# Kernel tuning notes

Hardware: AMD Instinct MI355X
Metric: run time of the kernel (lower is better)

## Reference

```python
import jax, jax.numpy as jnp
import numpy as np

N = 256    # num_neurons
I = 784    # input_dim
H = 128    # hidden_dim
B = 256    # batch
E = 4096   # num edges (sparse topology, fan_out 16)


def setup_inputs() -> dict:
    key = jax.random.key(0)
    k0, k1, k2, k3, k4 = jax.random.split(key, 5)
    x = jax.random.normal(k0, (B, I), dtype=jnp.float32)
    # per-neuron linear weights/biases (AutonomicNeuron modeled as Linear(input_dim, hidden_dim))
    W = jax.random.normal(k1, (N, I, H), dtype=jnp.float32) * (1.0 / np.sqrt(I))
    b = jax.random.normal(k2, (N, H), dtype=jnp.float32) * 0.01
    edge_index = jax.random.randint(k3, (2, E), 0, N)  # (2, E) [src; tgt]
    edge_weights = jax.random.normal(k4, (E,), dtype=jnp.float32) * 0.01  # init scale in _init_*_topology
    return {"x": x, "W": W, "b": b, "edge_index": edge_index, "edge_weights": edge_weights}


def reference(x, W, b, edge_index, edge_weights):
    # per-neuron projection: h0[n] = x @ W[n] + b[n]  -> (N, B, H)
    h0 = jnp.einsum('bi,nih->nbh', x, W) + b[:, None, :]
    src = edge_index[0]
    tgt = edge_index[1]
    # sequential, order-dependent message passing (faithful to the Python edge loop):
    # h[tgt] <- h[tgt] + h[src] * w, using the CURRENT h[src]
    def step(h, sw):
        s, t, w = sw
        h = h.at[t].add(h[s] * w)
        return h, None
    h_final, _ = jax.lax.scan(step, h0, (src, tgt, edge_weights))
    # aggregate: mean over all neurons' hidden states -> (B, H)
    return h_final.mean(axis=0)
```

## Files before the change

### kernel.cpp

```cpp
#include <hip/hip_runtime.h>

#define EDGES 4096
#define NNODES 256

typedef unsigned short u16;

__global__ __launch_bounds__(256) void k1_coeff(const int* __restrict__ ei,
                                                const float* __restrict__ ew,
                                                float* __restrict__ c_out) {
    __shared__ __align__(16) char smem[59648];
    float* w_q    = (float*)(smem);
    u16*   s_e    = (u16*)  (smem + 16384);
    u16*   t_e    = (u16*)  (smem + 24576);
    float* rho    = (float*)(smem + 16384);
    u16*   id_q   = (u16*)  (smem + 32768);
    u16*   t_q    = (u16*)  (smem + 40960);
    float* sfx    = (float*)(smem + 32768);
    u16*   id_u   = (u16*)  (smem + 49152);
    u16*   start_q= (u16*)  (smem + 49152);
    int*   offs   = (int*)  (smem + 57344);
    int*   fillc  = (int*)  (smem + 58372);

    const int tid = threadIdx.x;

    for (int j = tid; j < EDGES; j += 256) {
        s_e[j] = (u16)ei[j];
        t_e[j] = (u16)ei[EDGES + j];
    }
    fillc[tid] = 0;
    __syncthreads();

    for (int j = tid; j < EDGES; j += 256) atomicAdd(&fillc[s_e[j]], 1);
    __syncthreads();

    if (tid == 0) offs[0] = 0;
    offs[tid + 1] = fillc[tid];
    __syncthreads();
    for (int d = 1; d < 256; d <<= 1) {
        int add = (tid >= d) ? offs[tid + 1 - d] : 0;
        __syncthreads();
        offs[tid + 1] += add;
        __syncthreads();
    }

    fillc[tid] = offs[tid];
    __syncthreads();

    for (int j = tid; j < EDGES; j += 256) {
        int pos = atomicAdd(&fillc[s_e[j]], 1);
        id_u[pos] = (u16)j;
    }
    __syncthreads();

    for (int j = tid; j < EDGES; j += 256) {
        int s = s_e[j];
        int lo = offs[s], hi = offs[s + 1];
        int rank = 0;
        for (int q = lo; q < hi; ++q) rank += (id_u[q] < j) ? 1 : 0;
        id_q[lo + rank] = (u16)j;
    }
    __syncthreads();

    for (int q = tid; q < EDGES; q += 256) {
        int e = id_q[q];
        w_q[q] = ew[e];
        t_q[q] = t_e[e];
    }
    __syncthreads();

    for (int q = tid; q < EDGES; q += 256) {
        int myid = id_q[q];
        int t = t_q[q];
        int lo = offs[t], hi = offs[t + 1];
        const int hi0 = hi;
        while (lo < hi) {
            int mid = (lo + hi) >> 1;
            if (id_q[mid] > myid) hi = mid; else lo = mid + 1;
        }
        start_q[q] = (lo < hi0) ? (u16)lo : (u16)0xFFFFu;
    }
    __syncthreads();

    for (int q = tid; q < EDGES; q += 256) rho[q] = 1.0f;
    __syncthreads();

    for (int pass = 0; pass < 5; ++pass) {
        for (int q = tid; q < EDGES; q += 256) sfx[q] = w_q[q] * rho[q];
        __syncthreads();
        {
            int lo = offs[tid], hi = offs[tid + 1];
            float run = 0.0f;
            for (int q = hi - 1; q >= lo; --q) { run += sfx[q]; sfx[q] = run; }
        }
        __syncthreads();
        for (int q = tid; q < EDGES; q += 256) {
            int st = start_q[q];
            rho[q] = 1.0f + ((st != 0xFFFF) ? sfx[st] : 0.0f);
        }
        __syncthreads();
    }

    {
        int lo = offs[tid], hi = offs[tid + 1];
        float acc = 0.0f;
        for (int q = lo; q < hi; ++q) acc += w_q[q] * rho[q];
        c_out[tid] = (1.0f + acc) * (1.0f / 256.0f);
    }
}

__global__ __launch_bounds__(256) void k2_wc(const float* __restrict__ W,
                                             const float* __restrict__ bvec,
                                             const float* __restrict__ c,
                                             float* __restrict__ Wc) {
    const int bx = blockIdx.x;
    const int p  = blockIdx.y;
    const int n0 = p * 32;

    if (bx == 98) {
        int tid = threadIdx.x;
        if (tid < 32) {
            const float4* b4 = (const float4*)bvec;
            float4 acc = make_float4(0.f, 0.f, 0.f, 0.f);
            #pragma unroll 8
            for (int n = 0; n < 32; ++n) {
                float cn = c[n0 + n];
                float4 v = b4[(n0 + n) * 32 + tid];
                acc.x += cn * v.x; acc.y += cn * v.y;
                acc.z += cn * v.z; acc.w += cn * v.w;
            }
            float* dst = Wc + 784 * 128 + tid * 4;
            atomicAdd(dst + 0, acc.x);
            atomicAdd(dst + 1, acc.y);
            atomicAdd(dst + 2, acc.z);
            atomicAdd(dst + 3, acc.w);
        }
        return;
    }

    const int j  = bx * 256 + threadIdx.x;
    const int i  = j >> 5;
    const int h4 = j & 31;
    const float4* W4 = (const float4*)W;
    float4 acc = make_float4(0.f, 0.f, 0.f, 0.f);
    #pragma unroll 8
    for (int n = 0; n < 32; ++n) {
        float cn = c[n0 + n];
        float4 v = W4[((size_t)(n0 + n) * 784 + i) * 32 + h4];
        acc.x += cn * v.x; acc.y += cn * v.y;
        acc.z += cn * v.z; acc.w += cn * v.w;
    }
    float* dst = Wc + i * 128 + h4 * 4;
    atomicAdd(dst + 0, acc.x);
    atomicAdd(dst + 1, acc.y);
    atomicAdd(dst + 2, acc.z);
    atomicAdd(dst + 3, acc.w);
}

__global__ __launch_bounds__(256) void k3_gemm(const float* __restrict__ x,
                                               const float* __restrict__ Wc,
                                               float* __restrict__ out) {
    const int bg = blockIdx.x;
    const int kc = blockIdx.y;
    const int i0 = kc * 49;
    __shared__ float xs[16][49];
    const int tid = threadIdx.x;

    for (int idx = tid; idx < 16 * 49; idx += 256) {
        int row = idx / 49, ii = idx - row * 49;
        xs[row][ii] = x[(bg * 16 + row) * 784 + i0 + ii];
    }
    __syncthreads();

    const int h  = tid & 127;
    const int bh = tid >> 7;
    float acc[8];
    #pragma unroll
    for (int j = 0; j < 8; ++j) acc[j] = 0.0f;

    #pragma unroll 7
    for (int ii = 0; ii < 49; ++ii) {
        float wv = Wc[(i0 + ii) * 128 + h];
        #pragma unroll
        for (int j = 0; j < 8; ++j) acc[j] += xs[bh * 8 + j][ii] * wv;
    }

    if (kc == 15) {
        float bch = Wc[784 * 128 + h];
        #pragma unroll
        for (int j = 0; j < 8; ++j) acc[j] += bch;
    }

    #pragma unroll
    for (int j = 0; j < 8; ++j)
        atomicAdd(&out[(bg * 16 + bh * 8 + j) * 128 + h], acc[j]);
}

extern "C" void kernel_launch(void* const* d_in, const int* in_sizes, int n_in,
                              void* d_out, int out_size, void* d_ws, size_t ws_size,
                              hipStream_t stream) {
    const float* x  = (const float*)d_in[0];
    const float* W  = (const float*)d_in[1];
    const float* bv = (const float*)d_in[2];
    const int*   ei = (const int*)d_in[3];
    const float* ew = (const float*)d_in[4];
    float* out = (float*)d_out;

    float* c_ws = (float*)d_ws;
    float* Wc   = (float*)d_ws + 256;

    hipMemsetAsync(out, 0, (size_t)256 * 128 * sizeof(float), stream);
    hipMemsetAsync(Wc, 0, (size_t)785 * 128 * sizeof(float), stream);

    k1_coeff<<<1, 256, 0, stream>>>(ei, ew, c_ws);
    k2_wc<<<dim3(99, 8), 256, 0, stream>>>(W, bv, c_ws, Wc);
    k3_gemm<<<dim3(16, 16), 256, 0, stream>>>(x, Wc, out);
}
```

Baseline: 219.5 us.

## Use wave-shuffle scan, wider neuron chunks in Wc reduction, split-free GEMM

The block-wide prefix scan over neuron edge counts becomes a single-wavefront shuffle scan, which removes many barriers. The Wc reduction kernel now handles 64 neurons per block with coefficients cached in shared memory, halving the atomic traffic. The final GEMM no longer splits K: each block holds 4 full x rows in shared memory and writes outputs directly, which drops the output memset and the atomics. The cost is fewer blocks in both kernels (396 and 64), so less parallelism for the memory-bound W read and the GEMM.

```diff
diff --git a/kernel.cpp b/kernel.cpp
--- a/kernel.cpp
+++ b/kernel.cpp
@@ -33,15 +33,24 @@
     for (int j = tid; j < EDGES; j += 256) atomicAdd(&fillc[s_e[j]], 1);
     __syncthreads();
 
-    if (tid == 0) offs[0] = 0;
-    offs[tid + 1] = fillc[tid];
-    __syncthreads();
-    for (int d = 1; d < 256; d <<= 1) {
-        int add = (tid >= d) ? offs[tid + 1 - d] : 0;
-        __syncthreads();
-        offs[tid + 1] += add;
-        __syncthreads();
-    }
+    if (tid < 64) {
+        int b0 = tid * 4;
+        int c0 = fillc[b0], c1 = fillc[b0 + 1], c2 = fillc[b0 + 2], c3 = fillc[b0 + 3];
+        int s  = c0 + c1 + c2 + c3;
+        int inc = s;
+        #pragma unroll
+        for (int d = 1; d < 64; d <<= 1) {
+            int v = __shfl_up(inc, d);
+            if (tid >= d) inc += v;
+        }
+        int excl = inc - s;
+        offs[b0]     = excl;
+        offs[b0 + 1] = excl + c0;
+        offs[b0 + 2] = excl + c0 + c1;
+        offs[b0 + 3] = excl + c0 + c1 + c2;
+        if (tid == 63) offs[256] = inc;
+    }
+    __syncthreads();
 
     fillc[tid] = offs[tid];
     __syncthreads();
@@ -108,22 +117,26 @@
     }
 }
 
-__global__ __launch_bounds__(256) void k2_wc(const float* __restrict__ W,
-                                             const float* __restrict__ bvec,
-                                             const float* __restrict__ c,
-                                             float* __restrict__ Wc) {
+__global__ __launch_bounds__(256, 4) void k2_wc(const float* __restrict__ W,
+                                                const float* __restrict__ bvec,
+                                                const float* __restrict__ c,
+                                                float* __restrict__ Wc) {
     const int bx = blockIdx.x;
     const int p  = blockIdx.y;
-    const int n0 = p * 32;
+    const int n0 = p * 64;
+    __shared__ float cs[64];
+
+    const int tid = threadIdx.x;
+    if (tid < 64) cs[tid] = c[n0 + tid];
+    __syncthreads();
 
     if (bx == 98) {
-        int tid = threadIdx.x;
         if (tid < 32) {
             const float4* b4 = (const float4*)bvec;
             float4 acc = make_float4(0.f, 0.f, 0.f, 0.f);
-            #pragma unroll 8
-            for (int n = 0; n < 32; ++n) {
-                float cn = c[n0 + n];
+            #pragma unroll 16
+            for (int n = 0; n < 64; ++n) {
+                float cn = cs[n];
                 float4 v = b4[(n0 + n) * 32 + tid];
                 acc.x += cn * v.x; acc.y += cn * v.y;
                 acc.z += cn * v.z; acc.w += cn * v.w;
@@ -137,15 +150,15 @@
         return;
     }
 
-    const int j  = bx * 256 + threadIdx.x;
+    const int j  = bx * 256 + tid;
     const int i  = j >> 5;
     const int h4 = j & 31;
-    const float4* W4 = (const float4*)W;
+    const float4* W4 = (const float4*)W + ((size_t)n0 * 784 + i) * 32 + h4;
     float4 acc = make_float4(0.f, 0.f, 0.f, 0.f);
-    #pragma unroll 8
-    for (int n = 0; n < 32; ++n) {
-        float cn = c[n0 + n];
-        float4 v = W4[((size_t)(n0 + n) * 784 + i) * 32 + h4];
+    #pragma unroll 16
+    for (int n = 0; n < 64; ++n) {
+        float cn = cs[n];
+        float4 v = W4[(size_t)n * (784 * 32)];
         acc.x += cn * v.x; acc.y += cn * v.y;
         acc.z += cn * v.z; acc.w += cn * v.w;
     }
@@ -159,40 +172,30 @@
 __global__ __launch_bounds__(256) void k3_gemm(const float* __restrict__ x,
                                                const float* __restrict__ Wc,
                                                float* __restrict__ out) {
-    const int bg = blockIdx.x;
-    const int kc = blockIdx.y;
-    const int i0 = kc * 49;
-    __shared__ float xs[16][49];
+    const int blk = blockIdx.x;
+    __shared__ float xs[4 * 784];
     const int tid = threadIdx.x;
 
-    for (int idx = tid; idx < 16 * 49; idx += 256) {
-        int row = idx / 49, ii = idx - row * 49;
-        xs[row][ii] = x[(bg * 16 + row) * 784 + i0 + ii];
-    }
-    __syncthreads();
-
-    const int h  = tid & 127;
-    const int bh = tid >> 7;
-    float acc[8];
-    #pragma unroll
-    for (int j = 0; j < 8; ++j) acc[j] = 0.0f;
-
-    #pragma unroll 7
-    for (int ii = 0; ii < 49; ++ii) {
-        float wv = Wc[(i0 + ii) * 128 + h];
-        #pragma unroll
-        for (int j = 0; j < 8; ++j) acc[j] += xs[bh * 8 + j][ii] * wv;
-    }
-
-    if (kc == 15) {
-        float bch = Wc[784 * 128 + h];
-        #pragma unroll
-        for (int j = 0; j < 8; ++j) acc[j] += bch;
-    }
-
-    #pragma unroll
-    for (int j = 0; j < 8; ++j)
-        atomicAdd(&out[(bg * 16 + bh * 8 + j) * 128 + h], acc[j]);
+    const float4* x4  = (const float4*)(x + (size_t)blk * 4 * 784);
+    float4*       xs4 = (float4*)xs;
+    for (int idx = tid; idx < 4 * 196; idx += 256) xs4[idx] = x4[idx];
+    __syncthreads();
+
+    const int h    = tid & 127;
+    const int half = tid >> 7;
+    const float* xr0 = xs + (half * 2) * 784;
+    const float* xr1 = xs + (half * 2 + 1) * 784;
+
+    float a0 = 0.f, a1 = 0.f;
+    #pragma unroll 8
+    for (int i = 0; i < 784; ++i) {
+        float wv = Wc[i * 128 + h];
+        a0 += xr0[i] * wv;
+        a1 += xr1[i] * wv;
+    }
+    float bch = Wc[784 * 128 + h];
+    out[(size_t)(blk * 4 + half * 2) * 128 + h]     = a0 + bch;
+    out[(size_t)(blk * 4 + half * 2 + 1) * 128 + h] = a1 + bch;
 }
 
 extern "C" void kernel_launch(void* const* d_in, const int* in_sizes, int n_in,
@@ -208,10 +211,8 @@
     float* c_ws = (float*)d_ws;
     float* Wc   = (float*)d_ws + 256;
 
-    hipMemsetAsync(out, 0, (size_t)256 * 128 * sizeof(float), stream);
     hipMemsetAsync(Wc, 0, (size_t)785 * 128 * sizeof(float), stream);
-
     k1_coeff<<<1, 256, 0, stream>>>(ei, ew, c_ws);
-    k2_wc<<<dim3(99, 8), 256, 0, stream>>>(W, bv, c_ws, Wc);
-    k3_gemm<<<dim3(16, 16), 256, 0, stream>>>(x, Wc, out);
-}
+    k2_wc<<<dim3(99, 4), 256, 0, stream>>>(W, bv, c_ws, Wc);
+    k3_gemm<<<64, 256, 0, stream>>>(x, Wc, out);
+}
```

New measurement: 237.0 us. +8.0%, slower.
